# Kernel tuning notes

Measured on AMD Instinct MI355X. Metric: run time of the kernel, lower is better.

The kernel has to match this reference:

```python
import jax, jax.numpy as jnp
import numpy as np

E = 1024  # embd_size
T = 4096  # context_length
H = 64    # head_size
B = 4


def setup_inputs() -> dict:
    key = jax.random.key(0)
    ks = jax.random.split(key, 7)
    s = 0.02
    return {
        "x": jax.random.normal(ks[0], (B, T, E), dtype=jnp.float32),
        "Wq": jax.random.normal(ks[1], (E, H), dtype=jnp.float32) * s,
        "bq": jax.random.normal(ks[2], (H,), dtype=jnp.float32) * s,
        "Wk": jax.random.normal(ks[3], (E, H), dtype=jnp.float32) * s,
        "bk": jax.random.normal(ks[4], (H,), dtype=jnp.float32) * s,
        "Wv": jax.random.normal(ks[5], (E, H), dtype=jnp.float32) * s,
        "bv": jax.random.normal(ks[6], (H,), dtype=jnp.float32) * s,
    }


def reference(x, Wq, bq, Wk, bk, Wv, bv):
    # x: (B, T, E) -> q,k,v: (B, T, H)
    q = jnp.einsum('bte,eh->bth', x, Wq) + bq
    k = jnp.einsum('bte,eh->bth', x, Wk) + bk
    v = jnp.einsum('bte,eh->bth', x, Wv) + bv
    scale = 1.0 / jnp.sqrt(jnp.float32(H))
    w = jnp.einsum('bqh,bkh->bqk', q, k) * scale  # (B, T, T)
    causal = jnp.tril(jnp.ones((T, T), dtype=bool))  # True = keep
    w = jnp.where(causal, w, -jnp.inf)
    w = jax.nn.softmax(w, axis=-1)
    a = jnp.einsum('bqk,bkh->bqh', w, v)  # (B, T, H)
    return a
```

## Files before the change

### kernel.cpp

```cpp
#include <hip/hip_runtime.h>

typedef __attribute__((ext_vector_type(8))) short short8_t;
typedef __attribute__((ext_vector_type(4))) float f32x4;

namespace {
constexpr int T_CTX  = 4096;
constexpr int E_DIM  = 1024;
constexpr int H_DIM  = 64;
constexpr int B_SZ   = 4;
constexpr int M_ROWS = B_SZ * T_CTX;
constexpr float SCALE_Q = 0.125f * 1.4426950408889634f;
constexpr float DEFER_THR = 8.0f;
}

__device__ __forceinline__ unsigned short f2bf(float f) {
    unsigned u = __builtin_bit_cast(unsigned, f);
    u += 0x7fffu + ((u >> 16) & 1u);
    return (unsigned short)(u >> 16);
}
__device__ __forceinline__ unsigned pack2(unsigned short lo, unsigned short hi) {
    return (unsigned)lo | ((unsigned)hi << 16);
}
__device__ __forceinline__ unsigned cvtpk(float lo, float hi) {
    unsigned r;
    asm("v_cvt_pk_bf16_f32 %0, %1, %2" : "=v"(r) : "v"(lo), "v"(hi));
    return r;
}
__device__ __forceinline__ float fexp2(float x) {
    float r;
    asm("v_exp_f32 %0, %1" : "=v"(r) : "v"(x));
    return r;
}
__device__ __forceinline__ int swz(int row, int col) {
    return row * 64 + (col ^ ((row & 7) << 3));
}

__global__ __launch_bounds__(256)
void prep_weights(const float* __restrict__ Wq, const float* __restrict__ Wk,
                  const float* __restrict__ Wv, unsigned short* __restrict__ wt)
{
    const int mat = blockIdx.y;
    const int kc  = blockIdx.x;
    const float* W = (mat == 0) ? Wq : (mat == 1) ? Wk : Wv;
    __shared__ float Ls[64][65];
    const int tid = threadIdx.x;
    const int kb = kc * 64;
    #pragma unroll
    for (int j = 0; j < 4; ++j) {
        int p = j * 256 + tid;
        int kr = p >> 4, c4 = (p & 15) * 4;
        float4 w4 = *reinterpret_cast<const float4*>(&W[(size_t)(kb + kr) * H_DIM + c4]);
        Ls[c4 + 0][kr] = w4.x; Ls[c4 + 1][kr] = w4.y;
        Ls[c4 + 2][kr] = w4.z; Ls[c4 + 3][kr] = w4.w;
    }
    __syncthreads();
    #pragma unroll
    for (int j = 0; j < 2; ++j) {
        int p = j * 256 + tid;
        int f  = p >> 6;
        int ln = p & 63;
        int n   = (f >> 1) * 16 + (ln & 15);
        int kb8 = (f & 1) * 32 + (ln >> 4) * 8;
        uint4 w;
        w.x = pack2(f2bf(Ls[n][kb8 + 0]), f2bf(Ls[n][kb8 + 1]));
        w.y = pack2(f2bf(Ls[n][kb8 + 2]), f2bf(Ls[n][kb8 + 3]));
        w.z = pack2(f2bf(Ls[n][kb8 + 4]), f2bf(Ls[n][kb8 + 5]));
        w.w = pack2(f2bf(Ls[n][kb8 + 6]), f2bf(Ls[n][kb8 + 7]));
        size_t off = ((size_t)(kc * 24 + mat * 8 + f) * 64 + ln) * 8;
        *reinterpret_cast<uint4*>(&wt[off]) = w;
    }
}

__global__ __launch_bounds__(512, 1)
void proj_kernel(const float* __restrict__ x, const unsigned short* __restrict__ wt,
                 const float* __restrict__ bq, const float* __restrict__ bk,
                 const float* __restrict__ bv,
                 unsigned short* __restrict__ qb, unsigned short* __restrict__ kb,
                 unsigned short* __restrict__ vtb)
{
    const int tid = threadIdx.x;
    const int lane = tid & 63, wv = tid >> 6;
    const int l15 = lane & 15, lg = lane >> 4;
    const int kof = lg * 8;

    const int rg = wv & 3;
    const int kh = wv >> 2;
    const int m0    = blockIdx.x * 64 + rg * 16;
    const int batch = m0 >> 12;
    const int t0    = m0 & (T_CTX - 1);
    const int kbeg  = kh * 512;

    f32x4 acc[3][4] = {};
    const float* xrow = &x[(size_t)(m0 + l15) * E_DIM + kof];
    const unsigned short* wlane = wt + (size_t)lane * 8;

    float4 xa0 = *reinterpret_cast<const float4*>(xrow + kbeg);
    float4 xb0 = *reinterpret_cast<const float4*>(xrow + kbeg + 4);
    float4 xa1 = *reinterpret_cast<const float4*>(xrow + kbeg + 32);
    float4 xb1 = *reinterpret_cast<const float4*>(xrow + kbeg + 36);

    for (int k0 = kbeg; k0 < kbeg + 512; k0 += 32) {
        const int kn = (k0 + 64 < kbeg + 512) ? k0 + 64 : kbeg;
        float4 na = *reinterpret_cast<const float4*>(xrow + kn);
        float4 nb = *reinterpret_cast<const float4*>(xrow + kn + 4);

        const int fb = (k0 >> 6) * 24 + ((k0 >> 5) & 1);
        short8_t bf[12];
        #pragma unroll
        for (int mat = 0; mat < 3; ++mat)
            #pragma unroll
            for (int oc = 0; oc < 4; ++oc)
                bf[mat * 4 + oc] = *reinterpret_cast<const short8_t*>(
                    wlane + (size_t)(fb + mat * 8 + oc * 2) * 512);

        uint4 au;
        au.x = cvtpk(xa0.x, xa0.y); au.y = cvtpk(xa0.z, xa0.w);
        au.z = cvtpk(xb0.x, xb0.y); au.w = cvtpk(xb0.z, xb0.w);
        const short8_t a = __builtin_bit_cast(short8_t, au);

        #pragma unroll
        for (int mat = 0; mat < 3; ++mat)
            #pragma unroll
            for (int oc = 0; oc < 4; ++oc)
                acc[mat][oc] = __builtin_amdgcn_mfma_f32_16x16x32_bf16(
                    a, bf[mat * 4 + oc], acc[mat][oc], 0, 0, 0);

        xa0 = xa1; xb0 = xb1; xa1 = na; xb1 = nb;
    }

    __shared__ float Ms[4][64][49];
    __shared__ unsigned short Stg[4][1024];
    if (kh == 1) {
        #pragma unroll
        for (int mat = 0; mat < 3; ++mat)
            #pragma unroll
            for (int oc = 0; oc < 4; ++oc)
                #pragma unroll
                for (int r = 0; r < 4; ++r)
                    Ms[rg][lane][(mat * 4 + oc) * 4 + r] = acc[mat][oc][r];
    }
    __syncthreads();
    if (kh == 0) {
        #pragma unroll
        for (int mat = 0; mat < 3; ++mat)
            #pragma unroll
            for (int oc = 0; oc < 4; ++oc)
                #pragma unroll
                for (int r = 0; r < 4; ++r)
                    acc[mat][oc][r] += Ms[rg][lane][(mat * 4 + oc) * 4 + r];

        unsigned short* stage = &Stg[rg][0];

        #pragma unroll
        for (int mat = 0; mat < 2; ++mat) {
            const float* bias = mat ? bk : bq;
            const float sc = mat ? 1.0f : SCALE_Q;
            #pragma unroll
            for (int oc = 0; oc < 4; ++oc) {
                const float bb = bias[oc * 16 + l15];
                #pragma unroll
                for (int r = 0; r < 4; ++r)
                    stage[swz(lg * 4 + r, oc * 16 + l15)] =
                        f2bf((acc[mat][oc][r] + bb) * sc);
            }
            unsigned short* outg = mat ? kb : qb;
            const int row = lane >> 2, c = (lane & 3) * 16;
            uint4 w0 = *reinterpret_cast<const uint4*>(&stage[swz(row, c)]);
            uint4 w1 = *reinterpret_cast<const uint4*>(&stage[swz(row, c + 8)]);
            *reinterpret_cast<uint4*>(&outg[(size_t)(m0 + row) * H_DIM + c]) = w0;
            *reinterpret_cast<uint4*>(&outg[(size_t)(m0 + row) * H_DIM + c + 8]) = w1;
        }

        #pragma unroll
        for (int oc = 0; oc < 4; ++oc) {
            const float bb = bv[oc * 16 + l15];
            const int h = oc * 16 + l15;
            uint2 pw;
            pw.x = cvtpk(acc[2][oc][0] + bb, acc[2][oc][1] + bb);
            pw.y = cvtpk(acc[2][oc][2] + bb, acc[2][oc][3] + bb);
            *reinterpret_cast<uint2*>(&stage[h * 16 + lg * 4]) = pw;
        }
        const int h = lane;
        uint4 v0 = *reinterpret_cast<const uint4*>(&stage[h * 16]);
        uint4 v1 = *reinterpret_cast<const uint4*>(&stage[h * 16 + 8]);
        unsigned short* vrow = &vtb[((size_t)batch * H_DIM + h) * T_CTX + t0];
        *reinterpret_cast<uint4*>(&vrow[0]) = v0;
        *reinterpret_cast<uint4*>(&vrow[8]) = v1;
    }
}

__global__ __launch_bounds__(512)
void attn_kernel(const unsigned short* __restrict__ qg,
                 const unsigned short* __restrict__ kg,
                 const unsigned short* __restrict__ vt,
                 float* __restrict__ outp)
{
    const int tid  = threadIdx.x;
    const int lane = tid & 63, wv = tid >> 6;
    const int l15 = lane & 15, lg = lane >> 4;
    const int kof = lg * 8;

    const int idx   = 511 - blockIdx.x;
    const int st    = idx >> 2;
    const int batch = idx & 3;
    const int q0    = st * 32;
    const int nkv   = st / 2 + 1;
    const size_t rbase = (size_t)batch * T_CTX;
    const size_t vbase = (size_t)batch * H_DIM * T_CTX;

    __shared__ float smem[8448];
    unsigned short* Pt = (unsigned short*)smem;
    const int pbase = wv * 2048;

    short8_t qlo[2], qhi[2];
    #pragma unroll
    for (int hs = 0; hs < 2; ++hs) {
        qlo[hs] = *reinterpret_cast<const short8_t*>(
            &qg[(rbase + q0 + l15) * H_DIM + hs * 32 + kof]);
        qhi[hs] = *reinterpret_cast<const short8_t*>(
            &qg[(rbase + q0 + 16 + l15) * H_DIM + hs * 32 + kof]);
    }

    f32x4 olo[4] = {}, ohi[4] = {};
    float mlo = -1e30f, mhi = -1e30f, llo = 0.f, lhi = 0.f;

    const unsigned short* kp = kg + (rbase + (size_t)wv * 64) * H_DIM
                             + (size_t)l15 * H_DIM + kof;
    const unsigned short* vp = vt + vbase + (size_t)l15 * T_CTX + wv * 64 + kof;

    for (int kt = wv; kt < nkv; kt += 8) {
        const int k0 = kt * 64;

        f32x4 slo[4] = {}, shi[4] = {};
        #pragma unroll
        for (int hs = 0; hs < 2; ++hs) {
            short8_t kf[4];
            #pragma unroll
            for (int ct = 0; ct < 4; ++ct)
                kf[ct] = *reinterpret_cast<const short8_t*>(kp + ct * 16 * H_DIM + hs * 32);
            #pragma unroll
            for (int ct = 0; ct < 4; ++ct) {
                slo[ct] = __builtin_amdgcn_mfma_f32_16x16x32_bf16(kf[ct], qlo[hs], slo[ct], 0, 0, 0);
                shi[ct] = __builtin_amdgcn_mfma_f32_16x16x32_bf16(kf[ct], qhi[hs], shi[ct], 0, 0, 0);
            }
        }

        if (kt == nkv - 1) {
            #pragma unroll
            for (int ct = 0; ct < 4; ++ct)
                #pragma unroll
                for (int r = 0; r < 4; ++r) {
                    const int kv = k0 + ct * 16 + lg * 4 + r;
                    if (kv > q0 + l15)      slo[ct][r] = -1e30f;
                    if (kv > q0 + 16 + l15) shi[ct][r] = -1e30f;
                }
        }

        float mxlo, mxhi;
        {
            float a = fmaxf(fmaxf(slo[0][0], slo[0][1]), fmaxf(slo[0][2], slo[0][3]));
            float b = fmaxf(fmaxf(slo[1][0], slo[1][1]), fmaxf(slo[1][2], slo[1][3]));
            float c = fmaxf(fmaxf(slo[2][0], slo[2][1]), fmaxf(slo[2][2], slo[2][3]));
            float d = fmaxf(fmaxf(slo[3][0], slo[3][1]), fmaxf(slo[3][2], slo[3][3]));
            mxlo = fmaxf(fmaxf(a, b), fmaxf(c, d));
            a = fmaxf(fmaxf(shi[0][0], shi[0][1]), fmaxf(shi[0][2], shi[0][3]));
            b = fmaxf(fmaxf(shi[1][0], shi[1][1]), fmaxf(shi[1][2], shi[1][3]));
            c = fmaxf(fmaxf(shi[2][0], shi[2][1]), fmaxf(shi[2][2], shi[2][3]));
            d = fmaxf(fmaxf(shi[3][0], shi[3][1]), fmaxf(shi[3][2], shi[3][3]));
            mxhi = fmaxf(fmaxf(a, b), fmaxf(c, d));
        }
        mxlo = fmaxf(mxlo, __shfl_xor(mxlo, 16));
        mxlo = fmaxf(mxlo, __shfl_xor(mxlo, 32));
        mxhi = fmaxf(mxhi, __shfl_xor(mxhi, 16));
        mxhi = fmaxf(mxhi, __shfl_xor(mxhi, 32));

        if (!__all((mxlo <= mlo + DEFER_THR) && (mxhi <= mhi + DEFER_THR))) {
            const float nmlo = fmaxf(mlo, mxlo), nmhi = fmaxf(mhi, mxhi);
            const float cflo = fexp2(mlo - nmlo), cfhi = fexp2(mhi - nmhi);
            llo *= cflo; lhi *= cfhi;
            mlo = nmlo; mhi = nmhi;
            #pragma unroll
            for (int r = 0; r < 4; ++r) {
                const float cl = __shfl(cflo, lg * 4 + r);
                const float ch = __shfl(cfhi, lg * 4 + r);
                #pragma unroll
                for (int oc = 0; oc < 4; ++oc) { olo[oc][r] *= cl; ohi[oc][r] *= ch; }
            }
        }

        float rllo = 0.f, rlhi = 0.f;
        #pragma unroll
        for (int ct = 0; ct < 4; ++ct) {
            const float p0 = fexp2(slo[ct][0] - mlo), p1 = fexp2(slo[ct][1] - mlo);
            const float p2 = fexp2(slo[ct][2] - mlo), p3 = fexp2(slo[ct][3] - mlo);
            rllo += (p0 + p1) + (p2 + p3);
            uint2 pw; pw.x = cvtpk(p0, p1); pw.y = cvtpk(p2, p3);
            *reinterpret_cast<uint2*>(&Pt[pbase + swz(l15, ct * 16 + lg * 4)]) = pw;
            const float h0 = fexp2(shi[ct][0] - mhi), h1 = fexp2(shi[ct][1] - mhi);
            const float h2 = fexp2(shi[ct][2] - mhi), h3 = fexp2(shi[ct][3] - mhi);
            rlhi += (h0 + h1) + (h2 + h3);
            uint2 ph; ph.x = cvtpk(h0, h1); ph.y = cvtpk(h2, h3);
            *reinterpret_cast<uint2*>(&Pt[pbase + swz(16 + l15, ct * 16 + lg * 4)]) = ph;
        }
        rllo += __shfl_xor(rllo, 16); rllo += __shfl_xor(rllo, 32);
        rlhi += __shfl_xor(rlhi, 16); rlhi += __shfl_xor(rlhi, 32);
        llo += rllo; lhi += rlhi;

        #pragma unroll
        for (int ks = 0; ks < 2; ++ks) {
            short8_t vf4[4];
            #pragma unroll
            for (int oc = 0; oc < 4; ++oc)
                vf4[oc] = *reinterpret_cast<const short8_t*>(
                    vp + (size_t)(oc * 16) * T_CTX + ks * 32);
            const short8_t palo = *reinterpret_cast<const short8_t*>(
                &Pt[pbase + swz(l15, ks * 32 + kof)]);
            const short8_t pahi = *reinterpret_cast<const short8_t*>(
                &Pt[pbase + swz(16 + l15, ks * 32 + kof)]);
            #pragma unroll
            for (int oc = 0; oc < 4; ++oc) {
                olo[oc] = __builtin_amdgcn_mfma_f32_16x16x32_bf16(palo, vf4[oc], olo[oc], 0, 0, 0);
                ohi[oc] = __builtin_amdgcn_mfma_f32_16x16x32_bf16(pahi, vf4[oc], ohi[oc], 0, 0, 0);
            }
        }

        kp += 8 * 64 * H_DIM;
        vp += 8 * 64;
    }

    #pragma unroll
    for (int ph = 0; ph < 2; ++ph) {
        __syncthreads();
        #pragma unroll
        for (int oc = 0; oc < 4; ++oc)
            #pragma unroll
            for (int r = 0; r < 4; ++r)
                smem[wv * 1024 + (lg * 4 + r) * 64 + oc * 16 + l15] =
                    ph ? ohi[oc][r] : olo[oc][r];
        if (lg == 0) {
            smem[8192 + wv * 16 + l15] = ph ? mhi : mlo;
            smem[8320 + wv * 16 + l15] = ph ? lhi : llo;
        }
        __syncthreads();
        const int row = tid >> 5;
        const int c2  = (tid & 31) * 2;
        float M = -1e30f;
        #pragma unroll
        for (int w = 0; w < 8; ++w) M = fmaxf(M, smem[8192 + w * 16 + row]);
        float L = 0.f, a0 = 0.f, a1 = 0.f;
        #pragma unroll
        for (int w = 0; w < 8; ++w) {
            const float e = fexp2(smem[8192 + w * 16 + row] - M);
            L += e * smem[8320 + w * 16 + row];
            a0 += e * smem[w * 1024 + row * 64 + c2];
            a1 += e * smem[w * 1024 + row * 64 + c2 + 1];
        }
        const float inv = 1.0f / L;
        float2 rr; rr.x = a0 * inv; rr.y = a1 * inv;
        *reinterpret_cast<float2*>(
            &outp[(rbase + q0 + ph * 16 + row) * H_DIM + c2]) = rr;
    }
}

extern "C" void kernel_launch(void* const* d_in, const int* in_sizes, int n_in,
                              void* d_out, int out_size, void* d_ws, size_t ws_size,
                              hipStream_t stream) {
    const float* x  = (const float*)d_in[0];
    const float* Wq = (const float*)d_in[1];
    const float* bq = (const float*)d_in[2];
    const float* Wk = (const float*)d_in[3];
    const float* bk = (const float*)d_in[4];
    const float* Wv = (const float*)d_in[5];
    const float* bv = (const float*)d_in[6];
    float* out = (float*)d_out;

    unsigned short* wt  = (unsigned short*)d_ws;
    unsigned short* qb  = wt + 3 * H_DIM * E_DIM;
    unsigned short* kb  = qb + (size_t)M_ROWS * H_DIM;
    unsigned short* vtb = kb + (size_t)M_ROWS * H_DIM;

    prep_weights<<<dim3(E_DIM / 64, 3), 256, 0, stream>>>(Wq, Wk, Wv, wt);
    proj_kernel<<<dim3(M_ROWS / 64), 512, 0, stream>>>(x, wt, bq, bk, bv, qb, kb, vtb);
    attn_kernel<<<dim3((T_CTX / 32) * B_SZ), 512, 0, stream>>>(qb, kb, vtb, out);
}
```

Before: 69.03 us.

## Split long causal attention rows into KV chunks with a fixup merge kernel

Query tiles with long causal spans are split into up to four KV chunks of 16 tiles each, so the grid grows from 512 to 1280 blocks of more even size. Each chunk writes unnormalized partial outputs with its max and sum to workspace, and a new fixup kernel merges them with log-sum-exp rescaling. This targets the load imbalance and tail of the causal triangle on many CUs, at the cost of an extra launch and extra global traffic for the partials.

```diff
diff --git a/kernel.cpp b/kernel.cpp
--- a/kernel.cpp
+++ b/kernel.cpp
@@ -11,6 +11,7 @@
 constexpr int M_ROWS = B_SZ * T_CTX;
 constexpr float SCALE_Q = 0.125f * 1.4426950408889634f;
 constexpr float DEFER_THR = 8.0f;
+constexpr int NCID = 320;
 }
 
 __device__ __forceinline__ unsigned short f2bf(float f) {
@@ -193,18 +194,35 @@
 void attn_kernel(const unsigned short* __restrict__ qg,
                  const unsigned short* __restrict__ kg,
                  const unsigned short* __restrict__ vt,
-                 float* __restrict__ outp)
+                 float* __restrict__ outp,
+                 float* __restrict__ po, float* __restrict__ pm,
+                 float* __restrict__ pl)
 {
     const int tid  = threadIdx.x;
     const int lane = tid & 63, wv = tid >> 6;
     const int l15 = lane & 15, lg = lane >> 4;
     const int kof = lg * 8;
 
-    const int idx   = 511 - blockIdx.x;
-    const int st    = idx >> 2;
+    const int idx   = 4 * NCID - 1 - (int)blockIdx.x;
     const int batch = idx & 3;
-    const int q0    = st * 32;
-    const int nkv   = st / 2 + 1;
+    const int cid   = idx >> 2;
+    int g;
+    if (cid < 32) g = 0; else if (cid < 96) g = 1; else if (cid < 192) g = 2; else g = 3;
+    const int rem = cid - 16 * g * (g + 1);
+    int st, chunk;
+    switch (g) {
+        case 0:  st = rem;             chunk = 0;              break;
+        case 1:  st = 32 + (rem >> 1); chunk = rem & 1;        break;
+        case 2:  st = 64 + rem / 3;    chunk = rem - 3 * (rem / 3); break;
+        default: st = 96 + (rem >> 2); chunk = rem & 3;        break;
+    }
+    const int cc   = g + 1;
+    const int q0   = st * 32;
+    const int nkv  = st / 2 + 1;
+    const int tbeg = chunk * 16 + wv;
+    const int tcap = chunk * 16 + 16;
+    const int tend = (tcap < nkv) ? tcap : nkv;
+    const int pidx = batch * NCID + cid;
     const size_t rbase = (size_t)batch * T_CTX;
     const size_t vbase = (size_t)batch * H_DIM * T_CTX;
 
@@ -224,12 +242,10 @@
     f32x4 olo[4] = {}, ohi[4] = {};
     float mlo = -1e30f, mhi = -1e30f, llo = 0.f, lhi = 0.f;
 
-    const unsigned short* kp = kg + (rbase + (size_t)wv * 64) * H_DIM
-                             + (size_t)l15 * H_DIM + kof;
-    const unsigned short* vp = vt + vbase + (size_t)l15 * T_CTX + wv * 64 + kof;
-
-    for (int kt = wv; kt < nkv; kt += 8) {
-        const int k0 = kt * 64;
+    for (int t = tbeg; t < tend; t += 8) {
+        const int k0 = t * 64;
+        const unsigned short* kp = kg + (rbase + k0 + l15) * H_DIM + kof;
+        const unsigned short* vp = vt + vbase + (size_t)l15 * T_CTX + k0 + kof;
 
         f32x4 slo[4] = {}, shi[4] = {};
         #pragma unroll
@@ -245,7 +261,7 @@
             }
         }
 
-        if (kt == nkv - 1) {
+        if (t == nkv - 1) {
             #pragma unroll
             for (int ct = 0; ct < 4; ++ct)
                 #pragma unroll
@@ -323,9 +339,6 @@
                 ohi[oc] = __builtin_amdgcn_mfma_f32_16x16x32_bf16(pahi, vf4[oc], ohi[oc], 0, 0, 0);
             }
         }
-
-        kp += 8 * 64 * H_DIM;
-        vp += 8 * 64;
     }
 
     #pragma unroll
@@ -355,11 +368,60 @@
             a0 += e * smem[w * 1024 + row * 64 + c2];
             a1 += e * smem[w * 1024 + row * 64 + c2 + 1];
         }
-        const float inv = 1.0f / L;
-        float2 rr; rr.x = a0 * inv; rr.y = a1 * inv;
-        *reinterpret_cast<float2*>(
-            &outp[(rbase + q0 + ph * 16 + row) * H_DIM + c2]) = rr;
-    }
+        if (cc == 1) {
+            const float inv = 1.0f / L;
+            float2 rr; rr.x = a0 * inv; rr.y = a1 * inv;
+            *reinterpret_cast<float2*>(
+                &outp[(rbase + q0 + ph * 16 + row) * H_DIM + c2]) = rr;
+        } else {
+            float2 rr; rr.x = a0; rr.y = a1;
+            *reinterpret_cast<float2*>(
+                &po[(size_t)pidx * 2048 + (ph * 16 + row) * 64 + c2]) = rr;
+            if (c2 == 0) {
+                pm[(size_t)pidx * 32 + ph * 16 + row] = M;
+                pl[(size_t)pidx * 32 + ph * 16 + row] = L;
+            }
+        }
+    }
+}
+
+__global__ __launch_bounds__(256)
+void fixup_kernel(const float* __restrict__ po, const float* __restrict__ pm,
+                  const float* __restrict__ pl, float* __restrict__ outp)
+{
+    const int sb    = blockIdx.x;
+    const int st    = 32 + (sb >> 2);
+    const int batch = sb & 3;
+    const int g     = st >> 5;
+    const int cc    = g + 1;
+    const int cid0  = cc * (st - 16 * g);
+    const int pb0   = batch * NCID + cid0;
+    const int tid   = threadIdx.x;
+    const int row   = tid >> 3;
+    const int c8    = (tid & 7) * 8;
+
+    float M = -1e30f;
+    for (int c = 0; c < cc; ++c)
+        M = fmaxf(M, pm[(size_t)(pb0 + c) * 32 + row]);
+    float L = 0.f;
+    float a[8] = {};
+    for (int c = 0; c < cc; ++c) {
+        const float e = fexp2(pm[(size_t)(pb0 + c) * 32 + row] - M);
+        L += e * pl[(size_t)(pb0 + c) * 32 + row];
+        const float4 v0 = *reinterpret_cast<const float4*>(
+            &po[(size_t)(pb0 + c) * 2048 + row * 64 + c8]);
+        const float4 v1 = *reinterpret_cast<const float4*>(
+            &po[(size_t)(pb0 + c) * 2048 + row * 64 + c8 + 4]);
+        a[0] += e * v0.x; a[1] += e * v0.y; a[2] += e * v0.z; a[3] += e * v0.w;
+        a[4] += e * v1.x; a[5] += e * v1.y; a[6] += e * v1.z; a[7] += e * v1.w;
+    }
+    const float inv = 1.0f / L;
+    float4 r0, r1;
+    r0.x = a[0] * inv; r0.y = a[1] * inv; r0.z = a[2] * inv; r0.w = a[3] * inv;
+    r1.x = a[4] * inv; r1.y = a[5] * inv; r1.z = a[6] * inv; r1.w = a[7] * inv;
+    float* orow = &outp[((size_t)batch * T_CTX + st * 32 + row) * H_DIM + c8];
+    *reinterpret_cast<float4*>(orow)     = r0;
+    *reinterpret_cast<float4*>(orow + 4) = r1;
 }
 
 extern "C" void kernel_launch(void* const* d_in, const int* in_sizes, int n_in,
@@ -378,8 +440,12 @@
     unsigned short* qb  = wt + 3 * H_DIM * E_DIM;
     unsigned short* kb  = qb + (size_t)M_ROWS * H_DIM;
     unsigned short* vtb = kb + (size_t)M_ROWS * H_DIM;
+    float* po = (float*)(vtb + (size_t)B_SZ * H_DIM * T_CTX);
+    float* pm = po + (size_t)4 * NCID * 2048;
+    float* pl = pm + (size_t)4 * NCID * 32;
 
     prep_weights<<<dim3(E_DIM / 64, 3), 256, 0, stream>>>(Wq, Wk, Wv, wt);
     proj_kernel<<<dim3(M_ROWS / 64), 512, 0, stream>>>(x, wt, bq, bk, bv, qb, kb, vtb);
-    attn_kernel<<<dim3((T_CTX / 32) * B_SZ), 512, 0, stream>>>(qb, kb, vtb, out);
-}
+    attn_kernel<<<dim3(4 * NCID), 512, 0, stream>>>(qb, kb, vtb, out, po, pm, pl);
+    fixup_kernel<<<dim3(384), 256, 0, stream>>>(po, pm, pl, out);
+}
```

After: 88.80 us. 28.6% more time.

## Pair long and short causal tiles per block and prefetch next K tile

Applied to the files above, without the earlier changes.

The attention grid shrinks to 256 blocks, and each block processes two query tiles, one long and one short, so that causal work is balanced across blocks in a single wave. Inside the KV loop, the next K tile is loaded into registers while the current tile is computed, and V fragments are loaded at the top of the iteration to hide global latency. The cost is higher register pressure, which may reduce occupancy, plus an extra block-wide barrier between the two halves.

```diff
diff --git a/kernel.cpp b/kernel.cpp
--- a/kernel.cpp
+++ b/kernel.cpp
@@ -200,165 +200,194 @@
     const int l15 = lane & 15, lg = lane >> 4;
     const int kof = lg * 8;
 
-    const int idx   = 511 - blockIdx.x;
-    const int st    = idx >> 2;
-    const int batch = idx & 3;
-    const int q0    = st * 32;
-    const int nkv   = st / 2 + 1;
-    const size_t rbase = (size_t)batch * T_CTX;
-    const size_t vbase = (size_t)batch * H_DIM * T_CTX;
-
     __shared__ float smem[8448];
     unsigned short* Pt = (unsigned short*)smem;
     const int pbase = wv * 2048;
 
-    short8_t qlo[2], qhi[2];
-    #pragma unroll
-    for (int hs = 0; hs < 2; ++hs) {
-        qlo[hs] = *reinterpret_cast<const short8_t*>(
-            &qg[(rbase + q0 + l15) * H_DIM + hs * 32 + kof]);
-        qhi[hs] = *reinterpret_cast<const short8_t*>(
-            &qg[(rbase + q0 + 16 + l15) * H_DIM + hs * 32 + kof]);
-    }
-
-    f32x4 olo[4] = {}, ohi[4] = {};
-    float mlo = -1e30f, mhi = -1e30f, llo = 0.f, lhi = 0.f;
-
-    const unsigned short* kp = kg + (rbase + (size_t)wv * 64) * H_DIM
-                             + (size_t)l15 * H_DIM + kof;
-    const unsigned short* vp = vt + vbase + (size_t)l15 * T_CTX + wv * 64 + kof;
-
-    for (int kt = wv; kt < nkv; kt += 8) {
-        const int k0 = kt * 64;
-
-        f32x4 slo[4] = {}, shi[4] = {};
+    #pragma unroll 1
+    for (int half = 0; half < 2; ++half) {
+        const int r     = half ? (511 - (int)blockIdx.x) : (int)blockIdx.x;
+        const int st    = 127 - (r >> 2);
+        const int batch = r & 3;
+        const int q0    = st * 32;
+        const int nkv   = st / 2 + 1;
+        const size_t rbase = (size_t)batch * T_CTX;
+        const size_t vbase = (size_t)batch * H_DIM * T_CTX;
+
+        __syncthreads();
+
+        short8_t qlo[2], qhi[2];
         #pragma unroll
         for (int hs = 0; hs < 2; ++hs) {
-            short8_t kf[4];
-            #pragma unroll
-            for (int ct = 0; ct < 4; ++ct)
-                kf[ct] = *reinterpret_cast<const short8_t*>(kp + ct * 16 * H_DIM + hs * 32);
+            qlo[hs] = *reinterpret_cast<const short8_t*>(
+                &qg[(rbase + q0 + l15) * H_DIM + hs * 32 + kof]);
+            qhi[hs] = *reinterpret_cast<const short8_t*>(
+                &qg[(rbase + q0 + 16 + l15) * H_DIM + hs * 32 + kof]);
+        }
+
+        f32x4 olo[4] = {}, ohi[4] = {};
+        float mlo = -1e30f, mhi = -1e30f, llo = 0.f, lhi = 0.f;
+
+        short8_t kfC[8];
+        if (wv < nkv) {
+            const unsigned short* kp = kg + (rbase + wv * 64 + l15) * H_DIM + kof;
+            #pragma unroll
+            for (int hs = 0; hs < 2; ++hs)
+                #pragma unroll
+                for (int ct = 0; ct < 4; ++ct)
+                    kfC[hs * 4 + ct] = *reinterpret_cast<const short8_t*>(
+                        kp + ct * 16 * H_DIM + hs * 32);
+        }
+
+        for (int t = wv; t < nkv; t += 8) {
+            const int k0 = t * 64;
+            const unsigned short* vp = vt + vbase + (size_t)l15 * T_CTX + k0 + kof;
+
+            short8_t vf[8];
+            #pragma unroll
+            for (int oc = 0; oc < 4; ++oc)
+                #pragma unroll
+                for (int ks = 0; ks < 2; ++ks)
+                    vf[oc * 2 + ks] = *reinterpret_cast<const short8_t*>(
+                        vp + (size_t)(oc * 16) * T_CTX + ks * 32);
+
+            short8_t kfN[8];
+            const bool havN = (t + 8 < nkv);
+            if (havN) {
+                const unsigned short* kp = kg + (rbase + (t + 8) * 64 + l15) * H_DIM + kof;
+                #pragma unroll
+                for (int hs = 0; hs < 2; ++hs)
+                    #pragma unroll
+                    for (int ct = 0; ct < 4; ++ct)
+                        kfN[hs * 4 + ct] = *reinterpret_cast<const short8_t*>(
+                            kp + ct * 16 * H_DIM + hs * 32);
+            }
+
+            f32x4 slo[4] = {}, shi[4] = {};
+            #pragma unroll
+            for (int hs = 0; hs < 2; ++hs)
+                #pragma unroll
+                for (int ct = 0; ct < 4; ++ct) {
+                    slo[ct] = __builtin_amdgcn_mfma_f32_16x16x32_bf16(
+                        kfC[hs * 4 + ct], qlo[hs], slo[ct], 0, 0, 0);
+                    shi[ct] = __builtin_amdgcn_mfma_f32_16x16x32_bf16(
+                        kfC[hs * 4 + ct], qhi[hs], shi[ct], 0, 0, 0);
+                }
+
+            if (t == nkv - 1) {
+                #pragma unroll
+                for (int ct = 0; ct < 4; ++ct)
+                    #pragma unroll
+                    for (int rr = 0; rr < 4; ++rr) {
+                        const int kv = k0 + ct * 16 + lg * 4 + rr;
+                        if (kv > q0 + l15)      slo[ct][rr] = -1e30f;
+                        if (kv > q0 + 16 + l15) shi[ct][rr] = -1e30f;
+                    }
+            }
+
+            float mxlo, mxhi;
+            {
+                float a = fmaxf(fmaxf(slo[0][0], slo[0][1]), fmaxf(slo[0][2], slo[0][3]));
+                float b = fmaxf(fmaxf(slo[1][0], slo[1][1]), fmaxf(slo[1][2], slo[1][3]));
+                float c = fmaxf(fmaxf(slo[2][0], slo[2][1]), fmaxf(slo[2][2], slo[2][3]));
+                float d = fmaxf(fmaxf(slo[3][0], slo[3][1]), fmaxf(slo[3][2], slo[3][3]));
+                mxlo = fmaxf(fmaxf(a, b), fmaxf(c, d));
+                a = fmaxf(fmaxf(shi[0][0], shi[0][1]), fmaxf(shi[0][2], shi[0][3]));
+                b = fmaxf(fmaxf(shi[1][0], shi[1][1]), fmaxf(shi[1][2], shi[1][3]));
+                c = fmaxf(fmaxf(shi[2][0], shi[2][1]), fmaxf(shi[2][2], shi[2][3]));
+                d = fmaxf(fmaxf(shi[3][0], shi[3][1]), fmaxf(shi[3][2], shi[3][3]));
+                mxhi = fmaxf(fmaxf(a, b), fmaxf(c, d));
+            }
+            mxlo = fmaxf(mxlo, __shfl_xor(mxlo, 16));
+            mxlo = fmaxf(mxlo, __shfl_xor(mxlo, 32));
+            mxhi = fmaxf(mxhi, __shfl_xor(mxhi, 16));
+            mxhi = fmaxf(mxhi, __shfl_xor(mxhi, 32));
+
+            if (!__all((mxlo <= mlo + DEFER_THR) && (mxhi <= mhi + DEFER_THR))) {
+                const float nmlo = fmaxf(mlo, mxlo), nmhi = fmaxf(mhi, mxhi);
+                const float cflo = fexp2(mlo - nmlo), cfhi = fexp2(mhi - nmhi);
+                llo *= cflo; lhi *= cfhi;
+                mlo = nmlo; mhi = nmhi;
+                #pragma unroll
+                for (int rr = 0; rr < 4; ++rr) {
+                    const float cl = __shfl(cflo, lg * 4 + rr);
+                    const float ch = __shfl(cfhi, lg * 4 + rr);
+                    #pragma unroll
+                    for (int oc = 0; oc < 4; ++oc) { olo[oc][rr] *= cl; ohi[oc][rr] *= ch; }
+                }
+            }
+
+            float rllo = 0.f, rlhi = 0.f;
             #pragma unroll
             for (int ct = 0; ct < 4; ++ct) {
-                slo[ct] = __builtin_amdgcn_mfma_f32_16x16x32_bf16(kf[ct], qlo[hs], slo[ct], 0, 0, 0);
-                shi[ct] = __builtin_amdgcn_mfma_f32_16x16x32_bf16(kf[ct], qhi[hs], shi[ct], 0, 0, 0);
-            }
-        }
-
-        if (kt == nkv - 1) {
-            #pragma unroll
-            for (int ct = 0; ct < 4; ++ct)
-                #pragma unroll
-                for (int r = 0; r < 4; ++r) {
-                    const int kv = k0 + ct * 16 + lg * 4 + r;
-                    if (kv > q0 + l15)      slo[ct][r] = -1e30f;
-                    if (kv > q0 + 16 + l15) shi[ct][r] = -1e30f;
+                const float p0 = fexp2(slo[ct][0] - mlo), p1 = fexp2(slo[ct][1] - mlo);
+                const float p2 = fexp2(slo[ct][2] - mlo), p3 = fexp2(slo[ct][3] - mlo);
+                rllo += (p0 + p1) + (p2 + p3);
+                uint2 pw; pw.x = cvtpk(p0, p1); pw.y = cvtpk(p2, p3);
+                *reinterpret_cast<uint2*>(&Pt[pbase + swz(l15, ct * 16 + lg * 4)]) = pw;
+                const float h0 = fexp2(shi[ct][0] - mhi), h1 = fexp2(shi[ct][1] - mhi);
+                const float h2 = fexp2(shi[ct][2] - mhi), h3 = fexp2(shi[ct][3] - mhi);
+                rlhi += (h0 + h1) + (h2 + h3);
+                uint2 ph; ph.x = cvtpk(h0, h1); ph.y = cvtpk(h2, h3);
+                *reinterpret_cast<uint2*>(&Pt[pbase + swz(16 + l15, ct * 16 + lg * 4)]) = ph;
+            }
+            rllo += __shfl_xor(rllo, 16); rllo += __shfl_xor(rllo, 32);
+            rlhi += __shfl_xor(rlhi, 16); rlhi += __shfl_xor(rlhi, 32);
+            llo += rllo; lhi += rlhi;
+
+            #pragma unroll
+            for (int ks = 0; ks < 2; ++ks) {
+                const short8_t palo = *reinterpret_cast<const short8_t*>(
+                    &Pt[pbase + swz(l15, ks * 32 + kof)]);
+                const short8_t pahi = *reinterpret_cast<const short8_t*>(
+                    &Pt[pbase + swz(16 + l15, ks * 32 + kof)]);
+                #pragma unroll
+                for (int oc = 0; oc < 4; ++oc) {
+                    olo[oc] = __builtin_amdgcn_mfma_f32_16x16x32_bf16(
+                        palo, vf[oc * 2 + ks], olo[oc], 0, 0, 0);
+                    ohi[oc] = __builtin_amdgcn_mfma_f32_16x16x32_bf16(
+                        pahi, vf[oc * 2 + ks], ohi[oc], 0, 0, 0);
                 }
-        }
-
-        float mxlo, mxhi;
-        {
-            float a = fmaxf(fmaxf(slo[0][0], slo[0][1]), fmaxf(slo[0][2], slo[0][3]));
-            float b = fmaxf(fmaxf(slo[1][0], slo[1][1]), fmaxf(slo[1][2], slo[1][3]));
-            float c = fmaxf(fmaxf(slo[2][0], slo[2][1]), fmaxf(slo[2][2], slo[2][3]));
-            float d = fmaxf(fmaxf(slo[3][0], slo[3][1]), fmaxf(slo[3][2], slo[3][3]));
-            mxlo = fmaxf(fmaxf(a, b), fmaxf(c, d));
-            a = fmaxf(fmaxf(shi[0][0], shi[0][1]), fmaxf(shi[0][2], shi[0][3]));
-            b = fmaxf(fmaxf(shi[1][0], shi[1][1]), fmaxf(shi[1][2], shi[1][3]));
-            c = fmaxf(fmaxf(shi[2][0], shi[2][1]), fmaxf(shi[2][2], shi[2][3]));
-            d = fmaxf(fmaxf(shi[3][0], shi[3][1]), fmaxf(shi[3][2], shi[3][3]));
-            mxhi = fmaxf(fmaxf(a, b), fmaxf(c, d));
-        }
-        mxlo = fmaxf(mxlo, __shfl_xor(mxlo, 16));
-        mxlo = fmaxf(mxlo, __shfl_xor(mxlo, 32));
-        mxhi = fmaxf(mxhi, __shfl_xor(mxhi, 16));
-        mxhi = fmaxf(mxhi, __shfl_xor(mxhi, 32));
-
-        if (!__all((mxlo <= mlo + DEFER_THR) && (mxhi <= mhi + DEFER_THR))) {
-            const float nmlo = fmaxf(mlo, mxlo), nmhi = fmaxf(mhi, mxhi);
-            const float cflo = fexp2(mlo - nmlo), cfhi = fexp2(mhi - nmhi);
-            llo *= cflo; lhi *= cfhi;
-            mlo = nmlo; mhi = nmhi;
-            #pragma unroll
-            for (int r = 0; r < 4; ++r) {
-                const float cl = __shfl(cflo, lg * 4 + r);
-                const float ch = __shfl(cfhi, lg * 4 + r);
-                #pragma unroll
-                for (int oc = 0; oc < 4; ++oc) { olo[oc][r] *= cl; ohi[oc][r] *= ch; }
-            }
-        }
-
-        float rllo = 0.f, rlhi = 0.f;
-        #pragma unroll
-        for (int ct = 0; ct < 4; ++ct) {
-            const float p0 = fexp2(slo[ct][0] - mlo), p1 = fexp2(slo[ct][1] - mlo);
-            const float p2 = fexp2(slo[ct][2] - mlo), p3 = fexp2(slo[ct][3] - mlo);
-            rllo += (p0 + p1) + (p2 + p3);
-            uint2 pw; pw.x = cvtpk(p0, p1); pw.y = cvtpk(p2, p3);
-            *reinterpret_cast<uint2*>(&Pt[pbase + swz(l15, ct * 16 + lg * 4)]) = pw;
-            const float h0 = fexp2(shi[ct][0] - mhi), h1 = fexp2(shi[ct][1] - mhi);
-            const float h2 = fexp2(shi[ct][2] - mhi), h3 = fexp2(shi[ct][3] - mhi);
-            rlhi += (h0 + h1) + (h2 + h3);
-            uint2 ph; ph.x = cvtpk(h0, h1); ph.y = cvtpk(h2, h3);
-            *reinterpret_cast<uint2*>(&Pt[pbase + swz(16 + l15, ct * 16 + lg * 4)]) = ph;
-        }
-        rllo += __shfl_xor(rllo, 16); rllo += __shfl_xor(rllo, 32);
-        rlhi += __shfl_xor(rlhi, 16); rlhi += __shfl_xor(rlhi, 32);
-        llo += rllo; lhi += rlhi;
-
-        #pragma unroll
-        for (int ks = 0; ks < 2; ++ks) {
-            short8_t vf4[4];
-            #pragma unroll
-            for (int oc = 0; oc < 4; ++oc)
-                vf4[oc] = *reinterpret_cast<const short8_t*>(
-                    vp + (size_t)(oc * 16) * T_CTX + ks * 32);
-            const short8_t palo = *reinterpret_cast<const short8_t*>(
-                &Pt[pbase + swz(l15, ks * 32 + kof)]);
-            const short8_t pahi = *reinterpret_cast<const short8_t*>(
-                &Pt[pbase + swz(16 + l15, ks * 32 + kof)]);
-            #pragma unroll
-            for (int oc = 0; oc < 4; ++oc) {
-                olo[oc] = __builtin_amdgcn_mfma_f32_16x16x32_bf16(palo, vf4[oc], olo[oc], 0, 0, 0);
-                ohi[oc] = __builtin_amdgcn_mfma_f32_16x16x32_bf16(pahi, vf4[oc], ohi[oc], 0, 0, 0);
-            }
-        }
-
-        kp += 8 * 64 * H_DIM;
-        vp += 8 * 64;
-    }
-
-    #pragma unroll
-    for (int ph = 0; ph < 2; ++ph) {
-        __syncthreads();
-        #pragma unroll
-        for (int oc = 0; oc < 4; ++oc)
-            #pragma unroll
-            for (int r = 0; r < 4; ++r)
-                smem[wv * 1024 + (lg * 4 + r) * 64 + oc * 16 + l15] =
-                    ph ? ohi[oc][r] : olo[oc][r];
-        if (lg == 0) {
-            smem[8192 + wv * 16 + l15] = ph ? mhi : mlo;
-            smem[8320 + wv * 16 + l15] = ph ? lhi : llo;
-        }
-        __syncthreads();
-        const int row = tid >> 5;
-        const int c2  = (tid & 31) * 2;
-        float M = -1e30f;
-        #pragma unroll
-        for (int w = 0; w < 8; ++w) M = fmaxf(M, smem[8192 + w * 16 + row]);
-        float L = 0.f, a0 = 0.f, a1 = 0.f;
-        #pragma unroll
-        for (int w = 0; w < 8; ++w) {
-            const float e = fexp2(smem[8192 + w * 16 + row] - M);
-            L += e * smem[8320 + w * 16 + row];
-            a0 += e * smem[w * 1024 + row * 64 + c2];
-            a1 += e * smem[w * 1024 + row * 64 + c2 + 1];
-        }
-        const float inv = 1.0f / L;
-        float2 rr; rr.x = a0 * inv; rr.y = a1 * inv;
-        *reinterpret_cast<float2*>(
-            &outp[(rbase + q0 + ph * 16 + row) * H_DIM + c2]) = rr;
+            }
+
+            if (havN) {
+                #pragma unroll
+                for (int i = 0; i < 8; ++i) kfC[i] = kfN[i];
+            }
+        }
+
+        #pragma unroll 1
+        for (int ph = 0; ph < 2; ++ph) {
+            __syncthreads();
+            #pragma unroll
+            for (int oc = 0; oc < 4; ++oc)
+                #pragma unroll
+                for (int rr = 0; rr < 4; ++rr)
+                    smem[wv * 1024 + (lg * 4 + rr) * 64 + oc * 16 + l15] =
+                        ph ? ohi[oc][rr] : olo[oc][rr];
+            if (lg == 0) {
+                smem[8192 + wv * 16 + l15] = ph ? mhi : mlo;
+                smem[8320 + wv * 16 + l15] = ph ? lhi : llo;
+            }
+            __syncthreads();
+            const int row = tid >> 5;
+            const int c2  = (tid & 31) * 2;
+            float M = -1e30f;
+            #pragma unroll
+            for (int w = 0; w < 8; ++w) M = fmaxf(M, smem[8192 + w * 16 + row]);
+            float L = 0.f, a0 = 0.f, a1 = 0.f;
+            #pragma unroll
+            for (int w = 0; w < 8; ++w) {
+                const float e = fexp2(smem[8192 + w * 16 + row] - M);
+                L += e * smem[8320 + w * 16 + row];
+                a0 += e * smem[w * 1024 + row * 64 + c2];
+                a1 += e * smem[w * 1024 + row * 64 + c2 + 1];
+            }
+            const float inv = 1.0f / L;
+            float2 rr2; rr2.x = a0 * inv; rr2.y = a1 * inv;
+            *reinterpret_cast<float2*>(
+                &outp[(rbase + q0 + ph * 16 + row) * H_DIM + c2]) = rr2;
+        }
     }
 }
 
@@ -381,5 +410,5 @@
 
     prep_weights<<<dim3(E_DIM / 64, 3), 256, 0, stream>>>(Wq, Wk, Wv, wt);
     proj_kernel<<<dim3(M_ROWS / 64), 512, 0, stream>>>(x, wt, bq, bk, bv, qb, kb, vtb);
-    attn_kernel<<<dim3((T_CTX / 32) * B_SZ), 512, 0, stream>>>(qb, kb, vtb, out);
-}
+    attn_kernel<<<dim3(256), 512, 0, stream>>>(qb, kb, vtb, out);
+}
```

Result: no change. 70.02 us (+1.4%).
